# Kernel optimization log

Hardware: AMD Instinct MI355X
Metric: run time of the kernel (lower is better)

Reference implementation:

```python
import jax, jax.numpy as jnp
import numpy as np

B = 65536
HID = 256
C_K, C_V, C_S, NQ = 4, 8, 4, 4
EMB_OUT = 64  # state_embedding_size - 1


def _spatial_basis():
    # h = w = 5, U = V = 2 -> [5,5,4] Fourier basis
    ph = jnp.arange(1.0, 6.0)[:, None] * jnp.ones((1, 5)) * (np.pi / 5.0)
    pw = jnp.ones((5, 1)) * jnp.arange(1.0, 6.0)[None, :] * (np.pi / 5.0)
    u = jnp.arange(1.0, 3.0)[None, :]
    a = jnp.cos(ph[:, :, None] * u)  # [5,5,2]
    b = jnp.cos(pw[:, :, None] * u)  # [5,5,2]
    return jnp.einsum('hwu,hwv->hwuv', a, b).reshape(5, 5, 4).astype(jnp.float32)


def _conv(x, w, b):
    # x: NHWC, w: HWIO, pad=1, stride=1
    y = jax.lax.conv_general_dilated(x, w, window_strides=(1, 1), padding=[(1, 1), (1, 1)],
                                     dimension_numbers=('NHWC', 'HWIO', 'NHWC'))
    return y + b


def setup_inputs() -> dict:
    key = jax.random.key(0)
    ks = jax.random.split(key, 20)
    s = 0.05
    inp = {
        'X': jax.random.normal(ks[0], (B, 7, 7, 3), jnp.float32),
        'upper_module_hidden_state': jax.random.normal(ks[1], (B, HID), jnp.float32),
        'c1_w': jax.random.normal(ks[2], (5, 5, 3, 8), jnp.float32) * s,
        'c1_b': jax.random.normal(ks[3], (8,), jnp.float32) * s,
        'c2_w': jax.random.normal(ks[4], (3, 3, 8, 12), jnp.float32) * s,
        'c2_b': jax.random.normal(ks[5], (12,), jnp.float32) * s,
    }
    qdims = [(HID, 256), (256, 128), (128, 64), (64, 32), (32, 32)]
    for i, (din, dout) in enumerate(qdims):
        inp[f'qw{i}'] = jax.random.normal(ks[6 + 2 * i], (din, dout), jnp.float32) * s
        inp[f'qb{i}'] = jax.random.normal(ks[7 + 2 * i], (dout,), jnp.float32) * s
    inp['aw0'] = jax.random.normal(ks[16], ((C_V + C_S) * NQ, 32), jnp.float32) * s
    inp['ab0'] = jax.random.normal(ks[17], (32,), jnp.float32) * s
    inp['aw1'] = jax.random.normal(ks[18], (32, EMB_OUT), jnp.float32) * s
    inp['ab1'] = jax.random.normal(ks[19], (EMB_OUT,), jnp.float32) * s
    return inp


def reference(X, upper_module_hidden_state, c1_w, c1_b, c2_w, c2_b,
              qw0, qb0, qw1, qb1, qw2, qb2, qw3, qb3, qw4, qb4,
              aw0, ab0, aw1, ab1):
    b = X.shape[0]
    # vision CNN: [b,7,7,3] -> [b,5,5,8] -> [b,5,5,12]
    O = _conv(_conv(X, c1_w, c1_b), c2_w, c2_b)
    K, V = O[..., :C_K], O[..., C_K:]
    S = jnp.broadcast_to(_spatial_basis(), (b, 5, 5, C_S))
    K = jnp.concatenate([K, S], axis=-1)  # [b,5,5,8]
    V = jnp.concatenate([V, S], axis=-1)  # [b,5,5,12]
    # query MLP -> [b,4,8]
    q = upper_module_hidden_state
    for w, bi in [(qw0, qb0), (qw1, qb1), (qw2, qb2), (qw3, qb3)]:
        q = jax.nn.relu(q @ w + bi)
    q = (q @ qw4 + qb4).reshape(-1, NQ, C_K + C_S)
    # attention logits over 25 spatial positions, softmax over space
    A = jnp.einsum('bhwk,bqk->bhwq', K, q).reshape(b, 25, NQ)
    A = jax.nn.softmax(A, axis=1)
    # apply_alpha: [b,nq,25] @ [b,25,12] -> [b,nq,12]; chunk+cat == reshape
    a = jnp.einsum('bpq,bpd->bqd', A, V.reshape(b, 25, C_V + C_S)).reshape(b, NQ * (C_V + C_S))
    # answer MLP
    return jax.nn.relu(a @ aw0 + ab0) @ aw1 + ab1
```

## Files before the change

### kernel.cpp

```cpp
#include <hip/hip_runtime.h>
#include <hip/hip_bf16.h>

#define NB 65536

typedef __attribute__((ext_vector_type(8))) short short8;
typedef __attribute__((ext_vector_type(4))) short short4v;
typedef __attribute__((ext_vector_type(4))) float f32x4;
typedef __attribute__((ext_vector_type(16))) float f32x16;
typedef __attribute__((ext_vector_type(4))) unsigned int u32x4;

__device__ inline short f2bf(float f) {
    unsigned u = __builtin_bit_cast(unsigned, f);
    unsigned r = (u + 0x7fffu + ((u >> 16) & 1u)) >> 16;
    return (short)(unsigned short)r;
}
__device__ inline float b2f(short s) {
    return __builtin_bit_cast(float, (unsigned)((unsigned short)s) << 16);
}
__device__ inline unsigned pkbf(float lo, float hi) {
    return ((unsigned)(unsigned short)f2bf(hi) << 16) | (unsigned)(unsigned short)f2bf(lo);
}

#define MLPW_CNT 109568
#define WEFF_CNT 51200
#define A0 (MLPW_CNT + WEFF_CNT + 320)
#define A1 (A0 + 2048)
#define A2 (A1 + 2048)
#define A3 (A2 + 100)
#define PREP_TOT (A3 + 512)

__global__ void __launch_bounds__(256) prep_kernel(
    const float* __restrict__ w0, const float* __restrict__ w1,
    const float* __restrict__ w2, const float* __restrict__ w3,
    const float* __restrict__ w4,
    const float* __restrict__ b0, const float* __restrict__ b1,
    const float* __restrict__ b2, const float* __restrict__ b3,
    const float* __restrict__ b4,
    const float* __restrict__ c1w, const float* __restrict__ c1b,
    const float* __restrict__ c2w, const float* __restrict__ c2b,
    const float* __restrict__ aw0, const float* __restrict__ aw1,
    short* __restrict__ wt, short* __restrict__ weff, float* __restrict__ beff,
    short* __restrict__ aw0T, short* __restrict__ aw1T, float* __restrict__ sTab,
    float* __restrict__ biasP)
{
    int idx = blockIdx.x * 256 + threadIdx.x;
    if (idx < MLPW_CNT) {
        const float* W; int N, KT, base;
        if (idx < 65536)       { W = w0; N = 256; KT = 16; base = 0; }
        else if (idx < 98304)  { W = w1; N = 128; KT = 16; base = 65536; }
        else if (idx < 106496) { W = w2; N = 64;  KT = 8;  base = 98304; }
        else if (idx < 108544) { W = w3; N = 32;  KT = 4;  base = 106496; }
        else                   { W = w4; N = 32;  KT = 2;  base = 108544; }
        int i  = idx - base;
        int nt = i / (KT * 512);
        int r1 = i - nt * (KT * 512);
        int kt = r1 >> 9;
        int l  = (r1 & 511) >> 3;
        int j  = i & 7;
        int n  = nt * 32 + (l & 31);
        int k  = kt * 16 + ((l >> 5) << 3) + j;
        wt[idx] = f2bf(W[k * N + n]);
    } else if (idx < MLPW_CNT + WEFF_CNT) {
        int it = idx - MLPW_CNT;
        int n = it / 160, k = it - n * 160;
        float acc = 0.f;
        if (n < 300 && k < 147) {
            int oc = n % 12, p = n / 12, oy = p / 5, ox = p - oy * 5;
            int ci = k % 3,  t = k / 3, iy = t / 7, ix = t - iy * 7;
            for (int y = 0; y < 5; ++y) {
                int ky = iy - y + 1, ly = y - oy + 1;
                if ((unsigned)ky < 5u && (unsigned)ly < 3u) {
                    for (int x = 0; x < 5; ++x) {
                        int kx = ix - x + 1, lx = x - ox + 1;
                        if ((unsigned)kx < 5u && (unsigned)lx < 3u) {
                            const float* p1 = c1w + ((ky * 5 + kx) * 3 + ci) * 8;
                            const float* p2 = c2w + ((ly * 3 + lx) * 8) * 12 + oc;
#pragma unroll
                            for (int c = 0; c < 8; ++c) acc += p1[c] * p2[c * 12];
                        }
                    }
                }
            }
        }
        weff[it] = f2bf(acc);
    } else if (idx < A0) {
        int n = idx - MLPW_CNT - WEFF_CNT;
        float acc = 0.f;
        if (n < 300) {
            int oc = n % 12, p = n / 12, oy = p / 5, ox = p - oy * 5;
            acc = c2b[oc];
            for (int y = 0; y < 5; ++y) {
                int ly = y - oy + 1;
                if ((unsigned)ly < 3u) {
                    for (int x = 0; x < 5; ++x) {
                        int lx = x - ox + 1;
                        if ((unsigned)lx < 3u) {
#pragma unroll
                            for (int c = 0; c < 8; ++c)
                                acc += c2w[((ly * 3 + lx) * 8 + c) * 12 + oc] * c1b[c];
                        }
                    }
                }
            }
        }
        beff[n] = acc;
    } else if (idx < A1) {
        int t = idx - A0;
        int n = t >> 6, k = t & 63;
        aw0T[t] = (k < 48) ? f2bf(aw0[k * 32 + n]) : (short)0;
    } else if (idx < A2) {
        int t = idx - A1;
        int n = t >> 5, k = t & 31;
        aw1T[t] = f2bf(aw1[k * 64 + n]);
    } else if (idx < A3) {
        int i = idx - A2;
        int p = i >> 2, s = i & 3;
        int h = p / 5, w = p - 5 * h;
        int u = (s >> 1) + 1, v = (s & 1) + 1;
        const float PI5 = 0.6283185307179586f;
        sTab[i] = cosf(((float)(h + 1) * PI5) * (float)u) *
                  cosf(((float)(w + 1) * PI5) * (float)v);
    } else if (idx < PREP_TOT) {
        int t = idx - A3;
        const float* B; int N, base;
        if (t < 256)      { B = b0; N = 256; base = 0; }
        else if (t < 384) { B = b1; N = 128; base = 256; }
        else if (t < 448) { B = b2; N = 64;  base = 384; }
        else if (t < 480) { B = b3; N = 32;  base = 448; }
        else              { B = b4; N = 32;  base = 480; }
        int u  = t - base;
        int h  = u / (N / 2);
        int w  = u - h * (N / 2);
        int nt = w >> 4, r = w & 15;
        biasP[t] = B[nt * 32 + (r & 3) + 8 * (r >> 2) + 4 * h];
    }
}

template<int KT>
__device__ inline void stage_load(const short* __restrict__ src,
                                  short8* r, int tid)
{
    constexpr int CNT = (KT * 64 + 255) / 256;
#pragma unroll
    for (int i = 0; i < CNT; ++i) {
        int idx = tid + i * 256;
        if (idx < KT * 64) r[i] = *(const short8*)(src + idx * 8);
    }
}
template<int KT>
__device__ inline void stage_write(short* __restrict__ dst,
                                   const short8* r, int tid)
{
    constexpr int CNT = (KT * 64 + 255) / 256;
#pragma unroll
    for (int i = 0; i < CNT; ++i) {
        int idx = tid + i * 256;
        if (idx < KT * 64) *(short8*)(dst + idx * 8) = r[i];
    }
}

template<int K, int N, bool RELU>
__device__ inline void layerS(const short* __restrict__ wp,
                              const float* __restrict__ bp,
                              const u32x4* __restrict__ inF,
                              u32x4* __restrict__ outF,
                              short* __restrict__ sW0,
                              short* __restrict__ sW1,
                              int tid, int lane, int h)
{
    constexpr int KT = K / 16, NT = N / 32;
    constexpr int CNT = (KT * 64 + 255) / 256;
    short8 tmp[CNT];

    stage_load<KT>(wp, tmp, tid);
    stage_write<KT>(sW0, tmp, tid);
    __syncthreads();

#pragma unroll
    for (int nt = 0; nt < NT; ++nt) {
        short* cur = (nt & 1) ? sW1 : sW0;
        short* nxt = (nt & 1) ? sW0 : sW1;
        if (nt + 1 < NT) stage_load<KT>(wp + (nt + 1) * KT * 512, tmp, tid);

        f32x16 a;
#pragma unroll
        for (int r = 0; r < 16; ++r) a[r] = 0.f;
#pragma unroll
        for (int kt = 0; kt < KT; ++kt) {
            short8 wf = *(const short8*)(cur + kt * 512 + lane * 8);
            a = __builtin_amdgcn_mfma_f32_32x32x16_bf16(
                    wf, __builtin_bit_cast(short8, inF[kt]), a, 0, 0, 0);
        }
        const float* bpp = bp + h * (N / 2) + nt * 16;
        unsigned q[8];
#pragma unroll
        for (int i = 0; i < 8; ++i) {
            float v0 = a[2 * i] + bpp[2 * i];
            float v1 = a[2 * i + 1] + bpp[2 * i + 1];
            if (RELU) { v0 = fmaxf(v0, 0.f); v1 = fmaxf(v1, 0.f); }
            q[i] = pkbf(v0, v1);
        }
        unsigned xq[8];
#pragma unroll
        for (int i = 0; i < 8; ++i) xq[i] = (unsigned)__shfl_xor((int)q[i], 32, 64);
        u32x4 fa, fb;
        if (h == 0) {
            fa[0] = q[0];  fa[1] = q[1];  fa[2] = xq[0]; fa[3] = xq[1];
            fb[0] = q[4];  fb[1] = q[5];  fb[2] = xq[4]; fb[3] = xq[5];
        } else {
            fa[0] = xq[2]; fa[1] = xq[3]; fa[2] = q[2];  fa[3] = q[3];
            fb[0] = xq[6]; fb[1] = xq[7]; fb[2] = q[6];  fb[3] = q[7];
        }
        outF[2 * nt]     = fa;
        outF[2 * nt + 1] = fb;

        if (nt + 1 < NT) stage_write<KT>(nxt, tmp, tid);
        __syncthreads();
    }
}

template<int K>
__device__ inline void layerQ(const short* __restrict__ wp,
                              const float* __restrict__ bp,
                              const u32x4* __restrict__ inF,
                              short* __restrict__ qout,
                              int lane, int h, int r0)
{
    constexpr int KT = K / 16;
    f32x16 a;
#pragma unroll
    for (int r = 0; r < 16; ++r) a[r] = 0.f;
#pragma unroll
    for (int kt = 0; kt < KT; ++kt) {
        short8 wf = *(const short8*)(wp + kt * 512 + lane * 8);
        a = __builtin_amdgcn_mfma_f32_32x32x16_bf16(
                wf, __builtin_bit_cast(short8, inF[kt]), a, 0, 0, 0);
    }
    const float* bpp = bp + h * 16;
    short* qb = qout + (size_t)(r0 + (lane & 31)) * 32 + 4 * h;
    const int fo[8] = {0, 2, 8, 10, 16, 18, 24, 26};
#pragma unroll
    for (int i = 0; i < 8; ++i) {
        float v0 = a[2 * i] + bpp[2 * i];
        float v1 = a[2 * i + 1] + bpp[2 * i + 1];
        *(unsigned*)(qb + fo[i]) = pkbf(v0, v1);
    }
}

__global__ void __launch_bounds__(256, 2) mlp_kernel(
    const float* __restrict__ hid,
    const short* __restrict__ wp,
    const float* __restrict__ biasP,
    short* __restrict__ qout)
{
    __shared__ __align__(16) short sW0[8192];
    __shared__ __align__(16) short sW1[8192];

    const int tid  = threadIdx.x;
    const int lane = tid & 63;
    const int wv   = tid >> 6;
    const int h = lane >> 5, b = lane & 31;
    const int r0 = blockIdx.x * 128 + wv * 32;

    u32x4 A[16], B[16], C[8], D[4], E[2];
    const float* hb = hid + (size_t)(r0 + b) * 256 + h * 8;
#pragma unroll
    for (int kt = 0; kt < 16; ++kt) {
        float4 x = *(const float4*)(hb + kt * 16);
        float4 y = *(const float4*)(hb + kt * 16 + 4);
        u32x4 f;
        f[0] = pkbf(x.x, x.y); f[1] = pkbf(x.z, x.w);
        f[2] = pkbf(y.x, y.y); f[3] = pkbf(y.z, y.w);
        A[kt] = f;
    }
    layerS<256, 256, true>(wp,          biasP,       A, B, sW0, sW1, tid, lane, h);
    layerS<256, 128, true>(wp + 65536,  biasP + 256, B, C, sW0, sW1, tid, lane, h);
    layerS<128,  64, true>(wp + 98304,  biasP + 384, C, D, sW0, sW1, tid, lane, h);
    layerS< 64,  32, true>(wp + 106496, biasP + 448, D, E, sW0, sW1, tid, lane, h);
    layerQ< 32>           (wp + 108544, biasP + 480, E, qout, lane, h, r0);
}

__global__ void __launch_bounds__(256, 2) conv_attn_kernel(
    const float* __restrict__ Xg,
    const short* __restrict__ weffT,
    const float* __restrict__ beff,
    const short* __restrict__ aw0T, const float* __restrict__ ab0,
    const short* __restrict__ aw1T, const float* __restrict__ ab1,
    const float* __restrict__ sTab,
    const short* __restrict__ qb16,
    float* __restrict__ out)
{
    __shared__ __align__(16) short sPool[4][4800];

    const int tid    = threadIdx.x;
    const int w      = tid >> 6;
    const int lane   = tid & 63;
    const int lanelo = lane & 15;
    const int g      = lane >> 4;
    const int e0     = blockIdx.x * 64 + w * 16;

    short* sKc = &sPool[w][0];
    short* sVc = &sPool[w][1600];
    short* sAh = &sPool[w][0];
    short* sHh = &sPool[w][1024];

    const int elq = lane >> 2, qiq = lane & 3;
    short8 qv = *(const short8*)(qb16 + (size_t)(e0 + elq) * 32 + qiq * 8);

    short8 af[5];
    {
        const float* xr = Xg + (size_t)(e0 + lanelo) * 147;
        const int c0g = g * 8;
#pragma unroll
        for (int kt = 0; kt < 5; ++kt) {
            int c0 = kt * 32 + c0g;
            float v[8];
#pragma unroll
            for (int j = 0; j < 8; ++j) {
                int c = c0 + j;
                v[j] = (c < 147) ? xr[c] : 0.f;
            }
            u32x4 u;
            u[0] = pkbf(v[0], v[1]); u[1] = pkbf(v[2], v[3]);
            u[2] = pkbf(v[4], v[5]); u[3] = pkbf(v[6], v[7]);
            af[kt] = __builtin_bit_cast(short8, u);
        }
    }

    float bv[19];
#pragma unroll
    for (int nt = 0; nt < 19; ++nt) bv[nt] = beff[nt * 16 + lanelo];

    short8 bf[3][5];
    {
        const short* wb0 = weffT + lanelo * 160 + g * 8;
        const short* wb1 = weffT + (16 + lanelo) * 160 + g * 8;
#pragma unroll
        for (int kt = 0; kt < 5; ++kt) {
            bf[0][kt] = *(const short8*)(wb0 + kt * 32);
            bf[1][kt] = *(const short8*)(wb1 + kt * 32);
        }
    }
#pragma unroll
    for (int nt = 0; nt < 19; ++nt) {
        if (nt + 2 < 19) {
            const short* wb = weffT + ((nt + 2) * 16 + lanelo) * 160 + g * 8;
#pragma unroll
            for (int kt = 0; kt < 5; ++kt)
                bf[(nt + 2) % 3][kt] = *(const short8*)(wb + kt * 32);
        }
        f32x4 a; a[0] = 0.f; a[1] = 0.f; a[2] = 0.f; a[3] = 0.f;
#pragma unroll
        for (int kt = 0; kt < 5; ++kt)
            a = __builtin_amdgcn_mfma_f32_16x16x32_bf16(af[kt], bf[nt % 3][kt], a, 0, 0, 0);
        int n = nt * 16 + lanelo;
        if (n < 300) {
            int p = n / 12, c = n - p * 12;
#pragma unroll
            for (int j = 0; j < 4; ++j) {
                int el = g * 4 + j;
                float v = a[j] + bv[nt];
                if (c < 4) sKc[el * 100 + p * 4 + c]       = f2bf(v);
                else       sVc[el * 200 + p * 8 + (c - 4)] = f2bf(v);
            }
        }
    }

    {
        const int el = elq, qi = qiq;
        float qf[8];
#pragma unroll
        for (int i = 0; i < 8; ++i) qf[i] = b2f(qv[i]);

        float lg[25];
        float mx = -1e30f;
#pragma unroll
        for (int c = 0; c < 5; ++c) {
            short4v kv[5]; float4 sv[5];
#pragma unroll
            for (int i = 0; i < 5; ++i) {
                int p = c * 5 + i;
                kv[i] = *(const short4v*)(sKc + el * 100 + p * 4);
                sv[i] = *(const float4*)(sTab + p * 4);
            }
#pragma unroll
            for (int i = 0; i < 5; ++i) {
                float s = b2f(kv[i][0]) * qf[0] + b2f(kv[i][1]) * qf[1]
                        + b2f(kv[i][2]) * qf[2] + b2f(kv[i][3]) * qf[3]
                        + sv[i].x * qf[4] + sv[i].y * qf[5]
                        + sv[i].z * qf[6] + sv[i].w * qf[7];
                lg[c * 5 + i] = s;
                mx = fmaxf(mx, s);
            }
        }
        float sum = 0.f;
#pragma unroll
        for (int p = 0; p < 25; ++p) { lg[p] = __expf(lg[p] - mx); sum += lg[p]; }
        float inv = 1.f / sum;

        float o[12];
#pragma unroll
        for (int d = 0; d < 12; ++d) o[d] = 0.f;
#pragma unroll
        for (int c = 0; c < 5; ++c) {
            short4v v0[5], v1[5]; float4 sv[5];
#pragma unroll
            for (int i = 0; i < 5; ++i) {
                int p = c * 5 + i;
                v0[i] = *(const short4v*)(sVc + el * 200 + p * 8);
                v1[i] = *(const short4v*)(sVc + el * 200 + p * 8 + 4);
                sv[i] = *(const float4*)(sTab + p * 4);
            }
#pragma unroll
            for (int i = 0; i < 5; ++i) {
                float wgt = lg[c * 5 + i];
                o[0] += wgt * b2f(v0[i][0]); o[1] += wgt * b2f(v0[i][1]);
                o[2] += wgt * b2f(v0[i][2]); o[3] += wgt * b2f(v0[i][3]);
                o[4] += wgt * b2f(v1[i][0]); o[5] += wgt * b2f(v1[i][1]);
                o[6] += wgt * b2f(v1[i][2]); o[7] += wgt * b2f(v1[i][3]);
                o[8]  += wgt * sv[i].x; o[9]  += wgt * sv[i].y;
                o[10] += wgt * sv[i].z; o[11] += wgt * sv[i].w;
            }
        }
#pragma unroll
        for (int d = 0; d < 12; ++d) {
            int col = qi * 12 + d;
            int ch = col >> 3;
            sAh[el * 64 + ((ch ^ (el & 7)) << 3) + (col & 7)] = f2bf(o[d] * inv);
        }
#pragma unroll
        for (int z = 0; z < 4; ++z) {
            int col = 48 + qi * 4 + z;
            int ch = col >> 3;
            sAh[el * 64 + ((ch ^ (el & 7)) << 3) + (col & 7)] = 0;
        }
    }

    {
        short8 bw0a = *(const short8*)(aw0T + (0 * 16 + lanelo) * 64 + g * 8);
        short8 bw1a = *(const short8*)(aw0T + (0 * 16 + lanelo) * 64 + 32 + g * 8);
        short8 bw0b = *(const short8*)(aw0T + (1 * 16 + lanelo) * 64 + g * 8);
        short8 bw1b = *(const short8*)(aw0T + (1 * 16 + lanelo) * 64 + 32 + g * 8);
        float bba = ab0[lanelo];
        float bbb = ab0[16 + lanelo];

        short8 aa0, aa1;
        {
            int p0 = (0 * 4 + g) ^ (lanelo & 7);
            int p1 = (1 * 4 + g) ^ (lanelo & 7);
            aa0 = *(const short8*)(sAh + lanelo * 64 + p0 * 8);
            aa1 = *(const short8*)(sAh + lanelo * 64 + p1 * 8);
        }
        f32x4 h0; h0[0] = 0.f; h0[1] = 0.f; h0[2] = 0.f; h0[3] = 0.f;
        f32x4 h1 = h0;
        h0 = __builtin_amdgcn_mfma_f32_16x16x32_bf16(aa0, bw0a, h0, 0, 0, 0);
        h0 = __builtin_amdgcn_mfma_f32_16x16x32_bf16(aa1, bw1a, h0, 0, 0, 0);
        h1 = __builtin_amdgcn_mfma_f32_16x16x32_bf16(aa0, bw0b, h1, 0, 0, 0);
        h1 = __builtin_amdgcn_mfma_f32_16x16x32_bf16(aa1, bw1b, h1, 0, 0, 0);
#pragma unroll
        for (int j = 0; j < 4; ++j) {
            int row = g * 4 + j;
            int n0 = lanelo, n1 = 16 + lanelo;
            float va = fmaxf(h0[j] + bba, 0.f);
            float vb = fmaxf(h1[j] + bbb, 0.f);
            sHh[row * 32 + (((n0 >> 3) ^ (row & 3)) << 3) + (n0 & 7)] = f2bf(va);
            sHh[row * 32 + (((n1 >> 3) ^ (row & 3)) << 3) + (n1 & 7)] = f2bf(vb);
        }
    }

    {
        short8 bw[4]; float bb[4];
#pragma unroll
        for (int nt3 = 0; nt3 < 4; ++nt3) {
            int n = nt3 * 16 + lanelo;
            bw[nt3] = *(const short8*)(aw1T + n * 32 + g * 8);
            bb[nt3] = ab1[n];
        }
        short8 ah;
        {
            int ph = (g ^ (lanelo & 3));
            ah = *(const short8*)(sHh + lanelo * 32 + ph * 8);
        }
#pragma unroll
        for (int nt3 = 0; nt3 < 4; ++nt3) {
            int n = nt3 * 16 + lanelo;
            f32x4 oacc; oacc[0] = 0.f; oacc[1] = 0.f; oacc[2] = 0.f; oacc[3] = 0.f;
            oacc = __builtin_amdgcn_mfma_f32_16x16x32_bf16(ah, bw[nt3], oacc, 0, 0, 0);
#pragma unroll
            for (int j = 0; j < 4; ++j) {
                int el = g * 4 + j;
                out[((size_t)e0 + el) * 64 + n] = oacc[j] + bb[nt3];
            }
        }
    }
}


extern "C" void kernel_launch(void* const* d_in, const int* in_sizes, int n_in,
                              void* d_out, int out_size, void* d_ws, size_t ws_size,
                              hipStream_t stream)
{
    const float* X   = (const float*)d_in[0];
    const float* hid = (const float*)d_in[1];
    const float* c1w = (const float*)d_in[2];
    const float* c1b = (const float*)d_in[3];
    const float* c2w = (const float*)d_in[4];
    const float* c2b = (const float*)d_in[5];
    const float* qw0 = (const float*)d_in[6];
    const float* qb0 = (const float*)d_in[7];
    const float* qw1 = (const float*)d_in[8];
    const float* qb1 = (const float*)d_in[9];
    const float* qw2 = (const float*)d_in[10];
    const float* qb2 = (const float*)d_in[11];
    const float* qw3 = (const float*)d_in[12];
    const float* qb3 = (const float*)d_in[13];
    const float* qw4 = (const float*)d_in[14];
    const float* qb4 = (const float*)d_in[15];
    const float* aw0 = (const float*)d_in[16];
    const float* ab0 = (const float*)d_in[17];
    const float* aw1 = (const float*)d_in[18];
    const float* ab1 = (const float*)d_in[19];

    float* out   = (float*)d_out;
    short* qb16  = (short*)d_ws;
    short* wsW   = qb16 + (size_t)NB * 32;
    short* weffT = wsW + MLPW_CNT;
    float* beff  = (float*)(weffT + WEFF_CNT);
    short* aw0T  = (short*)(beff + 320);
    short* aw1T  = aw0T + 2048;
    float* sTab  = (float*)(aw1T + 2048);
    float* biasP = sTab + 100;

    hipLaunchKernelGGL(prep_kernel, dim3((PREP_TOT + 255) / 256), dim3(256), 0, stream,
                       qw0, qw1, qw2, qw3, qw4, qb0, qb1, qb2, qb3, qb4,
                       c1w, c1b, c2w, c2b, aw0, aw1,
                       wsW, weffT, beff, aw0T, aw1T, sTab, biasP);
    hipLaunchKernelGGL(mlp_kernel, dim3(NB / 128), dim3(256), 0, stream,
                       hid, wsW, biasP, qb16);
    hipLaunchKernelGGL(conv_attn_kernel, dim3(NB / 64), dim3(256), 0, stream,
                       X, weffT, beff, aw0T, ab0, aw1T, ab1, sTab, qb16, out);
}
```

Baseline: 74.51 us.

## Fuse query MLP into conv-attention kernel and pass queries via LDS

Merges the MLP kernel and the conv/attention kernel into one launch. Two of four waves per block compute the 5-layer query MLP, reading weights straight from global/L2 instead of staging them in shared memory, and write q into LDS. The other waves start the conv work concurrently, and a barrier comes before the attention step. This drops one launch and the global round trip for q. In exchange, half the waves carry the serial MLP work, which may cause load imbalance and higher register pressure, and every wave now re-reads weights from cache.

```diff
diff --git a/kernel.cpp b/kernel.cpp
--- a/kernel.cpp
+++ b/kernel.cpp
@@ -28,6 +28,7 @@
 #define A2 (A1 + 2048)
 #define A3 (A2 + 100)
 #define PREP_TOT (A3 + 512)
+
 
 __global__ void __launch_bounds__(256) prep_kernel(
     const float* __restrict__ w0, const float* __restrict__ w1,
@@ -136,58 +137,22 @@
     }
 }
 
-template<int KT>
-__device__ inline void stage_load(const short* __restrict__ src,
-                                  short8* r, int tid)
-{
-    constexpr int CNT = (KT * 64 + 255) / 256;
-#pragma unroll
-    for (int i = 0; i < CNT; ++i) {
-        int idx = tid + i * 256;
-        if (idx < KT * 64) r[i] = *(const short8*)(src + idx * 8);
-    }
-}
-template<int KT>
-__device__ inline void stage_write(short* __restrict__ dst,
-                                   const short8* r, int tid)
-{
-    constexpr int CNT = (KT * 64 + 255) / 256;
-#pragma unroll
-    for (int i = 0; i < CNT; ++i) {
-        int idx = tid + i * 256;
-        if (idx < KT * 64) *(short8*)(dst + idx * 8) = r[i];
-    }
-}
-
 template<int K, int N, bool RELU>
-__device__ inline void layerS(const short* __restrict__ wp,
+__device__ inline void layerR(const short* __restrict__ wp,
                               const float* __restrict__ bp,
                               const u32x4* __restrict__ inF,
                               u32x4* __restrict__ outF,
-                              short* __restrict__ sW0,
-                              short* __restrict__ sW1,
-                              int tid, int lane, int h)
+                              int lane, int h)
 {
     constexpr int KT = K / 16, NT = N / 32;
-    constexpr int CNT = (KT * 64 + 255) / 256;
-    short8 tmp[CNT];
-
-    stage_load<KT>(wp, tmp, tid);
-    stage_write<KT>(sW0, tmp, tid);
-    __syncthreads();
-
 #pragma unroll
     for (int nt = 0; nt < NT; ++nt) {
-        short* cur = (nt & 1) ? sW1 : sW0;
-        short* nxt = (nt & 1) ? sW0 : sW1;
-        if (nt + 1 < NT) stage_load<KT>(wp + (nt + 1) * KT * 512, tmp, tid);
-
         f32x16 a;
 #pragma unroll
         for (int r = 0; r < 16; ++r) a[r] = 0.f;
 #pragma unroll
         for (int kt = 0; kt < KT; ++kt) {
-            short8 wf = *(const short8*)(cur + kt * 512 + lane * 8);
+            short8 wf = *(const short8*)(wp + (nt * KT + kt) * 512 + lane * 8);
             a = __builtin_amdgcn_mfma_f32_32x32x16_bf16(
                     wf, __builtin_bit_cast(short8, inF[kt]), a, 0, 0, 0);
         }
@@ -213,18 +178,14 @@
         }
         outF[2 * nt]     = fa;
         outF[2 * nt + 1] = fb;
-
-        if (nt + 1 < NT) stage_write<KT>(nxt, tmp, tid);
-        __syncthreads();
     }
 }
 
 template<int K>
-__device__ inline void layerQ(const short* __restrict__ wp,
-                              const float* __restrict__ bp,
-                              const u32x4* __restrict__ inF,
-                              short* __restrict__ qout,
-                              int lane, int h, int r0)
+__device__ inline void layerQL(const short* __restrict__ wp,
+                               const float* __restrict__ bp,
+                               const u32x4* __restrict__ inF,
+                               short* qout, int lane, int h)
 {
     constexpr int KT = K / 16;
     f32x16 a;
@@ -237,7 +198,7 @@
                 wf, __builtin_bit_cast(short8, inF[kt]), a, 0, 0, 0);
     }
     const float* bpp = bp + h * 16;
-    short* qb = qout + (size_t)(r0 + (lane & 31)) * 32 + 4 * h;
+    short* qb = qout + (lane & 31) * 32 + 4 * h;
     const int fo[8] = {0, 2, 8, 10, 16, 18, 24, 26};
 #pragma unroll
     for (int i = 0; i < 8; ++i) {
@@ -247,65 +208,54 @@
     }
 }
 
-__global__ void __launch_bounds__(256, 2) mlp_kernel(
+__global__ void __launch_bounds__(256, 3) fused_kernel(
     const float* __restrict__ hid,
     const short* __restrict__ wp,
     const float* __restrict__ biasP,
-    short* __restrict__ qout)
-{
-    __shared__ __align__(16) short sW0[8192];
-    __shared__ __align__(16) short sW1[8192];
-
-    const int tid  = threadIdx.x;
-    const int lane = tid & 63;
-    const int wv   = tid >> 6;
-    const int h = lane >> 5, b = lane & 31;
-    const int r0 = blockIdx.x * 128 + wv * 32;
-
-    u32x4 A[16], B[16], C[8], D[4], E[2];
-    const float* hb = hid + (size_t)(r0 + b) * 256 + h * 8;
-#pragma unroll
-    for (int kt = 0; kt < 16; ++kt) {
-        float4 x = *(const float4*)(hb + kt * 16);
-        float4 y = *(const float4*)(hb + kt * 16 + 4);
-        u32x4 f;
-        f[0] = pkbf(x.x, x.y); f[1] = pkbf(x.z, x.w);
-        f[2] = pkbf(y.x, y.y); f[3] = pkbf(y.z, y.w);
-        A[kt] = f;
-    }
-    layerS<256, 256, true>(wp,          biasP,       A, B, sW0, sW1, tid, lane, h);
-    layerS<256, 128, true>(wp + 65536,  biasP + 256, B, C, sW0, sW1, tid, lane, h);
-    layerS<128,  64, true>(wp + 98304,  biasP + 384, C, D, sW0, sW1, tid, lane, h);
-    layerS< 64,  32, true>(wp + 106496, biasP + 448, D, E, sW0, sW1, tid, lane, h);
-    layerQ< 32>           (wp + 108544, biasP + 480, E, qout, lane, h, r0);
-}
-
-__global__ void __launch_bounds__(256, 2) conv_attn_kernel(
     const float* __restrict__ Xg,
     const short* __restrict__ weffT,
     const float* __restrict__ beff,
     const short* __restrict__ aw0T, const float* __restrict__ ab0,
     const short* __restrict__ aw1T, const float* __restrict__ ab1,
     const float* __restrict__ sTab,
-    const short* __restrict__ qb16,
     float* __restrict__ out)
 {
     __shared__ __align__(16) short sPool[4][4800];
+    __shared__ __align__(16) short sQ[2048];
 
     const int tid    = threadIdx.x;
     const int w      = tid >> 6;
     const int lane   = tid & 63;
     const int lanelo = lane & 15;
     const int g      = lane >> 4;
-    const int e0     = blockIdx.x * 64 + w * 16;
+    const int blkE0  = blockIdx.x * 64;
+    const int e0     = blkE0 + w * 16;
 
     short* sKc = &sPool[w][0];
     short* sVc = &sPool[w][1600];
     short* sAh = &sPool[w][0];
     short* sHh = &sPool[w][1024];
 
-    const int elq = lane >> 2, qiq = lane & 3;
-    short8 qv = *(const short8*)(qb16 + (size_t)(e0 + elq) * 32 + qiq * 8);
+    if (w < 2) {
+        const int h2 = lane >> 5, b2 = lane & 31;
+        const int r0g = blkE0 + w * 32;
+        u32x4 A[16], Bb[16], C[8], D[4], E[2];
+        const float* hb = hid + (size_t)(r0g + b2) * 256 + h2 * 8;
+#pragma unroll
+        for (int kt = 0; kt < 16; ++kt) {
+            float4 x = *(const float4*)(hb + kt * 16);
+            float4 y = *(const float4*)(hb + kt * 16 + 4);
+            u32x4 f;
+            f[0] = pkbf(x.x, x.y); f[1] = pkbf(x.z, x.w);
+            f[2] = pkbf(y.x, y.y); f[3] = pkbf(y.z, y.w);
+            A[kt] = f;
+        }
+        layerR<256, 256, true>(wp,          biasP,       A,  Bb, lane, h2);
+        layerR<256, 128, true>(wp + 65536,  biasP + 256, Bb, C,  lane, h2);
+        layerR<128,  64, true>(wp + 98304,  biasP + 384, C,  D,  lane, h2);
+        layerR< 64,  32, true>(wp + 106496, biasP + 448, D,  E,  lane, h2);
+        layerQL< 32>          (wp + 108544, biasP + 480, E,  sQ + w * 1024, lane, h2);
+    }
 
     short8 af[5];
     {
@@ -366,8 +316,11 @@
         }
     }
 
+    __syncthreads();
+
     {
-        const int el = elq, qi = qiq;
+        const int el = lane >> 2, qi = lane & 3;
+        short8 qv = *(const short8*)(sQ + (w * 16 + el) * 32 + qi * 8);
         float qf[8];
 #pragma unroll
         for (int i = 0; i < 8; ++i) qf[i] = b2f(qv[i]);
@@ -535,8 +488,7 @@
                        qw0, qw1, qw2, qw3, qw4, qb0, qb1, qb2, qb3, qb4,
                        c1w, c1b, c2w, c2b, aw0, aw1,
                        wsW, weffT, beff, aw0T, aw1T, sTab, biasP);
-    hipLaunchKernelGGL(mlp_kernel, dim3(NB / 128), dim3(256), 0, stream,
-                       hid, wsW, biasP, qb16);
-    hipLaunchKernelGGL(conv_attn_kernel, dim3(NB / 64), dim3(256), 0, stream,
-                       X, weffT, beff, aw0T, ab0, aw1T, ab1, sTab, qb16, out);
-}
+    hipLaunchKernelGGL(fused_kernel, dim3(NB / 64), dim3(256), 0, stream,
+                       hid, wsW, biasP, X, weffT, beff,
+                       aw0T, ab0, aw1T, ab1, sTab, out);
+}
```

Measured after the change: 122.4 us. +64.3%, slower.

## Halve elements per wave in conv-attention and split softmax across lane pairs

Applied to the files above, without the earlier changes.

The conv/attention kernel now handles 8 elements per wave instead of 16. Each MFMA tile's 16 rows duplicate the 8 input rows, and only the first half of the output rows is stored. The attention softmax is split across two lanes per (element, query), each covering alternating spatial positions, and partial max, sum and outputs are combined with xor shuffles. LDS per block is halved and launch bounds raised to 4 blocks per CU, aiming for more occupancy and fewer live registers per thread. The cost is wasted MFMA work, since half of each tile's rows are redundant, and twice as many weight-fragment loads per element.

```diff
diff --git a/kernel.cpp b/kernel.cpp
--- a/kernel.cpp
+++ b/kernel.cpp
@@ -280,7 +280,7 @@
     layerQ< 32>           (wp + 108544, biasP + 480, E, qout, lane, h, r0);
 }
 
-__global__ void __launch_bounds__(256, 2) conv_attn_kernel(
+__global__ void __launch_bounds__(256, 4) conv_attn_kernel(
     const float* __restrict__ Xg,
     const short* __restrict__ weffT,
     const float* __restrict__ beff,
@@ -290,26 +290,26 @@
     const short* __restrict__ qb16,
     float* __restrict__ out)
 {
-    __shared__ __align__(16) short sPool[4][4800];
+    __shared__ __align__(16) short sPool[4][2400];
 
     const int tid    = threadIdx.x;
     const int w      = tid >> 6;
     const int lane   = tid & 63;
     const int lanelo = lane & 15;
     const int g      = lane >> 4;
-    const int e0     = blockIdx.x * 64 + w * 16;
+    const int e0     = blockIdx.x * 32 + w * 8;
 
     short* sKc = &sPool[w][0];
-    short* sVc = &sPool[w][1600];
+    short* sVc = &sPool[w][800];
     short* sAh = &sPool[w][0];
-    short* sHh = &sPool[w][1024];
-
-    const int elq = lane >> 2, qiq = lane & 3;
+    short* sHh = &sPool[w][512];
+
+    const int elq = lane >> 3, qiq = (lane >> 1) & 3, hfq = lane & 1;
     short8 qv = *(const short8*)(qb16 + (size_t)(e0 + elq) * 32 + qiq * 8);
 
     short8 af[5];
     {
-        const float* xr = Xg + (size_t)(e0 + lanelo) * 147;
+        const float* xr = Xg + (size_t)(e0 + (lanelo & 7)) * 147;
         const int c0g = g * 8;
 #pragma unroll
         for (int kt = 0; kt < 5; ++kt) {
@@ -354,7 +354,7 @@
         for (int kt = 0; kt < 5; ++kt)
             a = __builtin_amdgcn_mfma_f32_16x16x32_bf16(af[kt], bf[nt % 3][kt], a, 0, 0, 0);
         int n = nt * 16 + lanelo;
-        if (n < 300) {
+        if (n < 300 && g < 2) {
             int p = n / 12, c = n - p * 12;
 #pragma unroll
             for (int j = 0; j < 4; ++j) {
@@ -367,72 +367,70 @@
     }
 
     {
-        const int el = elq, qi = qiq;
+        const int el = elq, qi = qiq, hf = hfq;
         float qf[8];
 #pragma unroll
         for (int i = 0; i < 8; ++i) qf[i] = b2f(qv[i]);
 
-        float lg[25];
+        float lg[13];
         float mx = -1e30f;
 #pragma unroll
-        for (int c = 0; c < 5; ++c) {
-            short4v kv[5]; float4 sv[5];
-#pragma unroll
-            for (int i = 0; i < 5; ++i) {
-                int p = c * 5 + i;
-                kv[i] = *(const short4v*)(sKc + el * 100 + p * 4);
-                sv[i] = *(const float4*)(sTab + p * 4);
-            }
-#pragma unroll
-            for (int i = 0; i < 5; ++i) {
-                float s = b2f(kv[i][0]) * qf[0] + b2f(kv[i][1]) * qf[1]
-                        + b2f(kv[i][2]) * qf[2] + b2f(kv[i][3]) * qf[3]
-                        + sv[i].x * qf[4] + sv[i].y * qf[5]
-                        + sv[i].z * qf[6] + sv[i].w * qf[7];
-                lg[c * 5 + i] = s;
+        for (int i = 0; i < 13; ++i) {
+            int p = hf + 2 * i;
+            if (p < 25) {
+                short4v kv = *(const short4v*)(sKc + el * 100 + p * 4);
+                float4 sv = *(const float4*)(sTab + p * 4);
+                float s = b2f(kv[0]) * qf[0] + b2f(kv[1]) * qf[1]
+                        + b2f(kv[2]) * qf[2] + b2f(kv[3]) * qf[3]
+                        + sv.x * qf[4] + sv.y * qf[5]
+                        + sv.z * qf[6] + sv.w * qf[7];
+                lg[i] = s;
                 mx = fmaxf(mx, s);
-            }
-        }
+            } else {
+                lg[i] = -1e30f;
+            }
+        }
+        mx = fmaxf(mx, __shfl_xor(mx, 1));
         float sum = 0.f;
 #pragma unroll
-        for (int p = 0; p < 25; ++p) { lg[p] = __expf(lg[p] - mx); sum += lg[p]; }
+        for (int i = 0; i < 13; ++i) { lg[i] = __expf(lg[i] - mx); sum += lg[i]; }
+        sum += __shfl_xor(sum, 1);
         float inv = 1.f / sum;
 
         float o[12];
 #pragma unroll
         for (int d = 0; d < 12; ++d) o[d] = 0.f;
 #pragma unroll
-        for (int c = 0; c < 5; ++c) {
-            short4v v0[5], v1[5]; float4 sv[5];
-#pragma unroll
-            for (int i = 0; i < 5; ++i) {
-                int p = c * 5 + i;
-                v0[i] = *(const short4v*)(sVc + el * 200 + p * 8);
-                v1[i] = *(const short4v*)(sVc + el * 200 + p * 8 + 4);
-                sv[i] = *(const float4*)(sTab + p * 4);
-            }
-#pragma unroll
-            for (int i = 0; i < 5; ++i) {
-                float wgt = lg[c * 5 + i];
-                o[0] += wgt * b2f(v0[i][0]); o[1] += wgt * b2f(v0[i][1]);
-                o[2] += wgt * b2f(v0[i][2]); o[3] += wgt * b2f(v0[i][3]);
-                o[4] += wgt * b2f(v1[i][0]); o[5] += wgt * b2f(v1[i][1]);
-                o[6] += wgt * b2f(v1[i][2]); o[7] += wgt * b2f(v1[i][3]);
-                o[8]  += wgt * sv[i].x; o[9]  += wgt * sv[i].y;
-                o[10] += wgt * sv[i].z; o[11] += wgt * sv[i].w;
-            }
-        }
-#pragma unroll
-        for (int d = 0; d < 12; ++d) {
-            int col = qi * 12 + d;
-            int ch = col >> 3;
-            sAh[el * 64 + ((ch ^ (el & 7)) << 3) + (col & 7)] = f2bf(o[d] * inv);
-        }
-#pragma unroll
-        for (int z = 0; z < 4; ++z) {
-            int col = 48 + qi * 4 + z;
-            int ch = col >> 3;
-            sAh[el * 64 + ((ch ^ (el & 7)) << 3) + (col & 7)] = 0;
+        for (int i = 0; i < 13; ++i) {
+            int p = hf + 2 * i;
+            if (p < 25) {
+                float wgt = lg[i];
+                short4v v0 = *(const short4v*)(sVc + el * 200 + p * 8);
+                short4v v1 = *(const short4v*)(sVc + el * 200 + p * 8 + 4);
+                float4 sv = *(const float4*)(sTab + p * 4);
+                o[0] += wgt * b2f(v0[0]); o[1] += wgt * b2f(v0[1]);
+                o[2] += wgt * b2f(v0[2]); o[3] += wgt * b2f(v0[3]);
+                o[4] += wgt * b2f(v1[0]); o[5] += wgt * b2f(v1[1]);
+                o[6] += wgt * b2f(v1[2]); o[7] += wgt * b2f(v1[3]);
+                o[8]  += wgt * sv.x; o[9]  += wgt * sv.y;
+                o[10] += wgt * sv.z; o[11] += wgt * sv.w;
+            }
+        }
+#pragma unroll
+        for (int d = 0; d < 12; ++d) o[d] += __shfl_xor(o[d], 1);
+        if (hf == 0) {
+#pragma unroll
+            for (int d = 0; d < 12; ++d) {
+                int col = qi * 12 + d;
+                int ch = col >> 3;
+                sAh[el * 64 + ((ch ^ (el & 7)) << 3) + (col & 7)] = f2bf(o[d] * inv);
+            }
+#pragma unroll
+            for (int z = 0; z < 4; ++z) {
+                int col = 48 + qi * 4 + z;
+                int ch = col >> 3;
+                sAh[el * 64 + ((ch ^ (el & 7)) << 3) + (col & 7)] = 0;
+            }
         }
     }
 
@@ -457,14 +455,16 @@
         h0 = __builtin_amdgcn_mfma_f32_16x16x32_bf16(aa1, bw1a, h0, 0, 0, 0);
         h1 = __builtin_amdgcn_mfma_f32_16x16x32_bf16(aa0, bw0b, h1, 0, 0, 0);
         h1 = __builtin_amdgcn_mfma_f32_16x16x32_bf16(aa1, bw1b, h1, 0, 0, 0);
-#pragma unroll
-        for (int j = 0; j < 4; ++j) {
-            int row = g * 4 + j;
-            int n0 = lanelo, n1 = 16 + lanelo;
-            float va = fmaxf(h0[j] + bba, 0.f);
-            float vb = fmaxf(h1[j] + bbb, 0.f);
-            sHh[row * 32 + (((n0 >> 3) ^ (row & 3)) << 3) + (n0 & 7)] = f2bf(va);
-            sHh[row * 32 + (((n1 >> 3) ^ (row & 3)) << 3) + (n1 & 7)] = f2bf(vb);
+        if (g < 2) {
+#pragma unroll
+            for (int j = 0; j < 4; ++j) {
+                int row = g * 4 + j;
+                int n0 = lanelo, n1 = 16 + lanelo;
+                float va = fmaxf(h0[j] + bba, 0.f);
+                float vb = fmaxf(h1[j] + bbb, 0.f);
+                sHh[row * 32 + (((n0 >> 3) ^ (row & 3)) << 3) + (n0 & 7)] = f2bf(va);
+                sHh[row * 32 + (((n1 >> 3) ^ (row & 3)) << 3) + (n1 & 7)] = f2bf(vb);
+            }
         }
     }
 
@@ -486,10 +486,12 @@
             int n = nt3 * 16 + lanelo;
             f32x4 oacc; oacc[0] = 0.f; oacc[1] = 0.f; oacc[2] = 0.f; oacc[3] = 0.f;
             oacc = __builtin_amdgcn_mfma_f32_16x16x32_bf16(ah, bw[nt3], oacc, 0, 0, 0);
-#pragma unroll
-            for (int j = 0; j < 4; ++j) {
-                int el = g * 4 + j;
-                out[((size_t)e0 + el) * 64 + n] = oacc[j] + bb[nt3];
+            if (g < 2) {
+#pragma unroll
+                for (int j = 0; j < 4; ++j) {
+                    int el = g * 4 + j;
+                    out[((size_t)e0 + el) * 64 + n] = oacc[j] + bb[nt3];
+                }
             }
         }
     }
@@ -537,6 +539,6 @@
                        wsW, weffT, beff, aw0T, aw1T, sTab, biasP);
     hipLaunchKernelGGL(mlp_kernel, dim3(NB / 128), dim3(256), 0, stream,
                        hid, wsW, biasP, qb16);
-    hipLaunchKernelGGL(conv_attn_kernel, dim3(NB / 64), dim3(256), 0, stream,
+    hipLaunchKernelGGL(conv_attn_kernel, dim3(NB / 32), dim3(256), 0, stream,
                        X, weffT, beff, aw0T, ab0, aw1T, ab1, sTab, qb16, out);
 }
```

Measured after the change: 132.2 us. 77.5% more time.

## Stage conv weight tiles through LDS with async global_load_lds double buffering

Applied to the files above, without the earlier changes.

Replaces the per-wave register-prefetched weight fragments for the fused conv GEMM with a block-shared double-buffered LDS staging area filled by global_load_lds, so the four waves share one copy of each weight tile instead of each loading it separately. This cuts register pressure, and the launch bounds are raised to allow three blocks per CU for more occupancy. In exchange it adds a block-wide barrier every N-tile iteration and more LDS per block, which could serialize the waves and limit the occupancy gain.

```diff
diff --git a/kernel.cpp b/kernel.cpp
--- a/kernel.cpp
+++ b/kernel.cpp
@@ -280,7 +280,10 @@
     layerQ< 32>           (wp + 108544, biasP + 480, E, qout, lane, h, r0);
 }
 
-__global__ void __launch_bounds__(256, 2) conv_attn_kernel(
+typedef __attribute__((address_space(1))) const void glb_v;
+typedef __attribute__((address_space(3))) void lds_v;
+
+__global__ void __launch_bounds__(256, 3) conv_attn_kernel(
     const float* __restrict__ Xg,
     const short* __restrict__ weffT,
     const float* __restrict__ beff,
@@ -291,6 +294,7 @@
     float* __restrict__ out)
 {
     __shared__ __align__(16) short sPool[4][4800];
+    __shared__ __align__(16) short sB[2][2560];
 
     const int tid    = threadIdx.x;
     const int w      = tid >> 6;
@@ -331,28 +335,34 @@
 #pragma unroll
     for (int nt = 0; nt < 19; ++nt) bv[nt] = beff[nt * 16 + lanelo];
 
-    short8 bf[3][5];
-    {
-        const short* wb0 = weffT + lanelo * 160 + g * 8;
-        const short* wb1 = weffT + (16 + lanelo) * 160 + g * 8;
+#define STAGE_B(NT_, BUF_)                                                     \
+    {                                                                          \
+        const short* src0 = weffT + ((NT_) * 16 + lanelo) * 160 + w * 32 + g * 8; \
+        __builtin_amdgcn_global_load_lds((glb_v*)src0,                         \
+            (lds_v*)(&sB[BUF_][w * 512]), 16, 0, 0);                           \
+        if (w == 0) {                                                          \
+            const short* src1 = weffT + ((NT_) * 16 + lanelo) * 160 + 4 * 32 + g * 8; \
+            __builtin_amdgcn_global_load_lds((glb_v*)src1,                     \
+                (lds_v*)(&sB[BUF_][4 * 512]), 16, 0, 0);                       \
+        }                                                                      \
+    }
+
+    STAGE_B(0, 0)
+    __syncthreads();
+
+#pragma unroll
+    for (int nt = 0; nt < 19; ++nt) {
+        const int cur = nt & 1;
+        if (nt + 1 < 19) {
+            if ((nt & 1) == 0) { STAGE_B(nt + 1, 1) }
+            else               { STAGE_B(nt + 1, 0) }
+        }
+        f32x4 a; a[0] = 0.f; a[1] = 0.f; a[2] = 0.f; a[3] = 0.f;
 #pragma unroll
         for (int kt = 0; kt < 5; ++kt) {
-            bf[0][kt] = *(const short8*)(wb0 + kt * 32);
-            bf[1][kt] = *(const short8*)(wb1 + kt * 32);
-        }
-    }
-#pragma unroll
-    for (int nt = 0; nt < 19; ++nt) {
-        if (nt + 2 < 19) {
-            const short* wb = weffT + ((nt + 2) * 16 + lanelo) * 160 + g * 8;
-#pragma unroll
-            for (int kt = 0; kt < 5; ++kt)
-                bf[(nt + 2) % 3][kt] = *(const short8*)(wb + kt * 32);
-        }
-        f32x4 a; a[0] = 0.f; a[1] = 0.f; a[2] = 0.f; a[3] = 0.f;
-#pragma unroll
-        for (int kt = 0; kt < 5; ++kt)
-            a = __builtin_amdgcn_mfma_f32_16x16x32_bf16(af[kt], bf[nt % 3][kt], a, 0, 0, 0);
+            short8 bfv = *(const short8*)(&sB[cur][kt * 512 + lane * 8]);
+            a = __builtin_amdgcn_mfma_f32_16x16x32_bf16(af[kt], bfv, a, 0, 0, 0);
+        }
         int n = nt * 16 + lanelo;
         if (n < 300) {
             int p = n / 12, c = n - p * 12;
@@ -364,7 +374,9 @@
                 else       sVc[el * 200 + p * 8 + (c - 4)] = f2bf(v);
             }
         }
-    }
+        __syncthreads();
+    }
+#undef STAGE_B
 
     {
         const int el = elq, qi = qiq;
```

New measurement: 73.40 us. About the same (-1.5%).
